# Kernel tuning notes

Measured on AMD Instinct MI355X. Metric: run time of the kernel, lower is better.

## Reference

```python
import jax, jax.numpy as jnp
import numpy as np

B, S, D, H = 16, 577, 768, 12  # batch, seq (24*24+1 cls), hidden, heads
WH, WW = 24, 24
HEAD = D // H
NUM_REL = (2 * WH - 1) * (2 * WW - 1) + 3  # 2212


def make_rel_pos_index(wh, ww):
    # mirrors TFData2VecVisionRelativePositionBias.get_position_index
    xx, yy = np.meshgrid(np.arange(wh), np.arange(ww))  # 'xy' indexing like tf.meshgrid
    coords = np.stack([yy, xx], axis=0).reshape(2, -1)  # [2, wh*ww]
    rel = coords[:, :, None] - coords[:, None, :]       # [2, N, N]
    rel = rel.transpose(1, 2, 0)                        # [N, N, 2]
    rx = (rel[:, :, 0] + wh - 1) * (2 * ww - 1)
    ry = rel[:, :, 1] + ww - 1
    idx = rx + ry                                       # [N, N]
    n = idx.shape[0]
    top = np.full((1, n), NUM_REL - 3, dtype=idx.dtype)
    left = np.full((n, 1), NUM_REL - 2, dtype=idx.dtype)
    corner = np.full((1, 1), NUM_REL - 1, dtype=idx.dtype)
    idx = np.concatenate([top, idx], axis=0)
    idx = np.concatenate([np.concatenate([corner, left], axis=0), idx], axis=1)
    return idx.astype(np.int32)  # [N+1, N+1]


def setup_inputs() -> dict:
    key = jax.random.key(0)
    ks = jax.random.split(key, 6)
    scale = 0.02
    return {
        "hidden_states": jax.random.normal(ks[0], (B, S, D), jnp.float32),
        "Wq": jax.random.normal(ks[1], (D, D), jnp.float32) * scale,
        "bq": jnp.zeros((D,), jnp.float32),
        "Wk": jax.random.normal(ks[2], (D, D), jnp.float32) * scale,
        "Wv": jax.random.normal(ks[3], (D, D), jnp.float32) * scale,
        "bv": jnp.zeros((D,), jnp.float32),
        "rel_pos_bias_table": jax.random.normal(ks[4], (NUM_REL, H), jnp.float32) * scale,
        "rel_pos_index": jnp.asarray(make_rel_pos_index(WH, WW)),
    }


def reference(hidden_states, Wq, bq, Wk, Wv, bv, rel_pos_bias_table, rel_pos_index):
    b, s, _ = hidden_states.shape
    q = (hidden_states @ Wq + bq).reshape(b, s, H, HEAD).transpose(0, 2, 1, 3)
    k = (hidden_states @ Wk).reshape(b, s, H, HEAD).transpose(0, 2, 1, 3)
    v = (hidden_states @ Wv + bv).reshape(b, s, H, HEAD).transpose(0, 2, 1, 3)
    scores = jnp.einsum("bhqd,bhkd->bhqk", q, k) / jnp.sqrt(jnp.float32(HEAD))
    # gathered relative position bias: [S, S, H] -> [H, S, S]
    bias = rel_pos_bias_table[rel_pos_index].transpose(2, 0, 1)
    scores = scores + bias[None]
    probs = jax.nn.softmax(scores, axis=-1)
    out = jnp.einsum("bhqk,bhkd->bhqd", probs, v)
    out = out.transpose(0, 2, 1, 3).reshape(b, s, D)
    return out
```

## Files before the change

kernel.cpp:

```cpp
#include <hip/hip_runtime.h>
#include <hip/hip_bf16.h>


typedef __attribute__((ext_vector_type(8))) short bf16x8;
typedef __attribute__((ext_vector_type(4))) float f32x4;
typedef unsigned short u16;

#define SEQ 577
#define MTOT 9232
#define QKV_STRIDE 7090176
#define VT_PITCH 640
#define B_PITCH 640

static __device__ __forceinline__ u16 f2bf(float x) {
  unsigned int u = __float_as_uint(x);
  u = (u + 0x7FFFu + ((u >> 16) & 1u)) >> 16;
  return (u16)u;
}
static __device__ __forceinline__ float bf2f(u16 v) {
  return __uint_as_float(((unsigned int)v) << 16);
}

static __device__ __forceinline__ void gload_lds16(const void* g, void* l) {
  __builtin_amdgcn_global_load_lds(
      (const __attribute__((address_space(1))) unsigned int*)g,
      (__attribute__((address_space(3))) unsigned int*)l, 16, 0, 0);
}

__global__ __launch_bounds__(256) void prep(
    const float* __restrict__ Wq, const float* __restrict__ Wk,
    const float* __restrict__ Wv, const float* __restrict__ X,
    u16* __restrict__ WT, u16* __restrict__ Xb) {
  const int bid = blockIdx.x;
  if (bid < 1728) {
    __shared__ float t[32][33];
    const int z = bid / 576;
    const int rem = bid - z * 576;
    const int kx = rem % 24, ny = rem / 24;
    const float* W = (z == 0) ? Wq : (z == 1) ? Wk : Wv;
    int x = threadIdx.x & 31;
    int y = threadIdx.x >> 5;
    int k0 = kx * 32;
    int n0 = ny * 32;
#pragma unroll
    for (int i = 0; i < 4; ++i)
      t[y + i * 8][x] = W[(size_t)(k0 + y + i * 8) * 768 + n0 + x];
    __syncthreads();
    u16* o = WT + (size_t)z * 589824;
#pragma unroll
    for (int i = 0; i < 4; ++i)
      o[(size_t)(n0 + y + i * 8) * 768 + k0 + x] = f2bf(t[x][y + i * 8]);
  } else {
    size_t i = ((size_t)(bid - 1728) * 256 + threadIdx.x) * 8;
    if (i >= (size_t)MTOT * 768) return;
    const float4* xp = (const float4*)(X + i);
    float4 a = xp[0], b = xp[1];
    u16 pk[8] = {f2bf(a.x), f2bf(a.y), f2bf(a.z), f2bf(a.w),
                 f2bf(b.x), f2bf(b.y), f2bf(b.z), f2bf(b.w)};
    *(int4*)(Xb + i) = *(const int4*)pk;
  }
}

__global__ __launch_bounds__(256) void prep2(
    const u16* __restrict__ v,
    u16* __restrict__ vT,
    const float* __restrict__ table, const int* __restrict__ idx,
    u16* __restrict__ biasm) {
  const int bid = blockIdx.x;
  const int tid = threadIdx.x;
  if (bid < 960) {
    const int tile = bid % 5;
    const int bh = bid / 5;
    const int b = bh / 12, h = bh % 12;
    __shared__ u16 T[128][64];
    const int s0 = tile * 128;
    const u16* vp = v + (size_t)b * SEQ * 768 + h * 64;
#pragma unroll
    for (int it = 0; it < 4; ++it) {
      int c = tid + it * 256;
      int r = c >> 3, ko = (c & 7) << 3;
      int gs = s0 + r;
      int4 val = make_int4(0, 0, 0, 0);
      if (gs < SEQ) val = *(const int4*)(vp + (size_t)gs * 768 + ko);
      *(int4*)&T[r][ko ^ (((r >> 3) & 7) << 3)] = val;
    }
    __syncthreads();
    u16* op = vT + (size_t)bh * 64 * VT_PITCH;
#pragma unroll
    for (int it = 0; it < 4; ++it) {
      int c = tid + it * 256;
      int d = c >> 4, so = (c & 15) << 3;
      u16 tmp[8];
#pragma unroll
      for (int j = 0; j < 8; ++j) {
        int rr = so + j;
        tmp[j] = T[rr][d ^ (((rr >> 3) & 7) << 3)];
      }
      *(int4*)(op + (size_t)d * VT_PITCH + s0 + so) = *(const int4*)tmp;
    }
  } else {
    const int r = bid - 960;
    const int q = r % 577;
    const int h = r / 577;
    for (int k = tid; k < B_PITCH; k += 256) {
      u16 vv = 0;
      if (k < SEQ) vv = f2bf(table[idx[q * SEQ + k] * 12 + h]);
      biasm[((size_t)h * SEQ + q) * B_PITCH + k] = vv;
    }
  }
}

#define STAGE_A(BUF, KT, MH)                                                   \
  do {                                                                         \
    gload_lds16(asrc[(MH)] + (KT) * 64, &TILES[(BUF)][0][(MH) * 64 + w8][0]);  \
    gload_lds16(asrc[(MH) + 2] + (KT) * 64,                                    \
                &TILES[(BUF)][0][128 + (MH) * 64 + w8][0]);                    \
  } while (0)

#define STAGE_B(BUF, KT, NH)                                                   \
  do {                                                                         \
    gload_lds16(bsrc + (size_t)((NH) * 32) * 768 + (KT) * 64,                  \
                &TILES[(BUF)][1][bw + (NH) * 32][0]);                          \
    gload_lds16(bsrc + (size_t)(128 + (NH) * 32) * 768 + (KT) * 64,            \
                &TILES[(BUF)][1][128 + bw + (NH) * 32][0]);                    \
  } while (0)

#define LOAD_A(BUF, MH)                                                        \
  do {                                                                         \
    const char* _p =                                                           \
        (const char*)&TILES[(BUF)][0][wm2 * 128 + (MH) * 64 + l15][0];         \
    af[0][0] = *(const bf16x8*)(_p + ca0);                                     \
    af[0][1] = *(const bf16x8*)(_p + ca1);                                     \
    af[1][0] = *(const bf16x8*)(_p + 2048 + ca0);                              \
    af[1][1] = *(const bf16x8*)(_p + 2048 + ca1);                              \
    af[2][0] = *(const bf16x8*)(_p + 4096 + ca0);                              \
    af[2][1] = *(const bf16x8*)(_p + 4096 + ca1);                              \
    af[3][0] = *(const bf16x8*)(_p + 6144 + ca0);                              \
    af[3][1] = *(const bf16x8*)(_p + 6144 + ca1);                              \
  } while (0)

#define LOAD_B(BUF, NH)                                                        \
  do {                                                                         \
    const char* _p =                                                           \
        (const char*)&TILES[(BUF)][1][wn * 64 + (NH) * 32 + l15][0];           \
    bfr[0][0] = *(const bf16x8*)(_p + ca0);                                    \
    bfr[0][1] = *(const bf16x8*)(_p + ca1);                                    \
    bfr[1][0] = *(const bf16x8*)(_p + 2048 + ca0);                             \
    bfr[1][1] = *(const bf16x8*)(_p + 2048 + ca1);                             \
  } while (0)

#define MFMA_Q(MH, NH)                                                         \
  do {                                                                         \
    _Pragma("unroll") for (int _i = 0; _i < 4; ++_i)                           \
        _Pragma("unroll") for (int _j = 0; _j < 2; ++_j)                       \
            acc[(MH) * 4 + _i][(NH) * 2 + _j] =                                \
        __builtin_amdgcn_mfma_f32_16x16x32_bf16(                               \
            af[_i][0], bfr[_j][0], acc[(MH) * 4 + _i][(NH) * 2 + _j], 0, 0,    \
            0);                                                                \
    _Pragma("unroll") for (int _i = 0; _i < 4; ++_i)                           \
        _Pragma("unroll") for (int _j = 0; _j < 2; ++_j)                       \
            acc[(MH) * 4 + _i][(NH) * 2 + _j] =                                \
        __builtin_amdgcn_mfma_f32_16x16x32_bf16(                               \
            af[_i][1], bfr[_j][1], acc[(MH) * 4 + _i][(NH) * 2 + _j], 0, 0,    \
            0);                                                                \
  } while (0)

#define PH_MID                                                                 \
  do {                                                                         \
    asm volatile("" ::: "memory");                                             \
    __builtin_amdgcn_s_barrier();                                              \
    asm volatile("s_waitcnt lgkmcnt(0)" ::: "memory");                         \
    __builtin_amdgcn_s_setprio(1);                                             \
  } while (0)

#define PH_END                                                                 \
  do {                                                                         \
    __builtin_amdgcn_s_setprio(0);                                             \
    asm volatile("" ::: "memory");                                             \
    __builtin_amdgcn_s_barrier();                                              \
    asm volatile("" ::: "memory");                                             \
  } while (0)

__global__ __launch_bounds__(512, 2) void qkv_gemm(
    const u16* __restrict__ Xb,
    const u16* __restrict__ WT,
    const float* __restrict__ bq, const float* __restrict__ bv,
    u16* __restrict__ qkv) {
  const int bid = blockIdx.x;
  const int xcd = bid & 7;
  const int r8 = bid >> 3;
  const int mt = (r8 / 9) * 8 + xcd;
  if (mt >= 37) return;
  const int nt = r8 % 9;
  const int m0 = mt * 256;
  const int widx = nt / 3;
  const int nb = (nt % 3) * 256;

  const int tid = threadIdx.x;
  const int lane = tid & 63;
  const int w = tid >> 6;
  const int wm2 = w >> 2;
  const int wn = w & 3;
  const int quad = lane >> 4;
  const int l15 = lane & 15;

  __shared__ u16 TILES[2][2][256][64];

  const int lr = lane >> 3;
  const int w8 = w * 8;
  const int ce = ((lane & 7) ^ lr) * 8;
  const u16* asrc[4];
#pragma unroll
  for (int c = 0; c < 4; ++c) {
    int rr = m0 + c * 64 + w8 + lr;
    if (rr > MTOT - 1) rr = MTOT - 1;
    asrc[c] = Xb + (size_t)rr * 768 + ce;
  }
  const int bw = (w >> 2) * 64 + (w & 3) * 8;
  const u16* bsrc = WT + (size_t)widx * 589824 + (size_t)(nb + bw + lr) * 768 + ce;

  const int lswz = (l15 & 7) << 4;
  const int ca0 = (quad * 16) ^ lswz;
  const int ca1 = ca0 ^ 64;

  f32x4 acc[8][4];
#pragma unroll
  for (int i = 0; i < 8; ++i)
#pragma unroll
    for (int j = 0; j < 4; ++j) acc[i][j] = (f32x4){0.f, 0.f, 0.f, 0.f};
  bf16x8 af[4][2], bfr[2][2];

  STAGE_A(0, 0, 0); STAGE_B(0, 0, 1); STAGE_A(0, 0, 1); STAGE_B(0, 0, 0);
  STAGE_A(1, 1, 0); STAGE_B(1, 1, 1); STAGE_A(1, 1, 1);
  asm volatile("s_waitcnt vmcnt(6)" ::: "memory");
  __builtin_amdgcn_s_barrier();
  asm volatile("" ::: "memory");

  for (int t = 0; t < 12; ++t) {
    const int buf = t & 1;
    const int nbuf = buf ^ 1;
    LOAD_A(buf, 0);
    LOAD_B(buf, 0);
    if (t <= 10) STAGE_B(nbuf, t + 1, 0);
    PH_MID; MFMA_Q(0, 0); PH_END;
    LOAD_B(buf, 1);
    if (t <= 9) STAGE_A(buf, t + 2, 0);
    PH_MID; MFMA_Q(0, 1); PH_END;
    LOAD_A(buf, 1);
    if (t <= 9) STAGE_B(buf, t + 2, 1);
    PH_MID; MFMA_Q(1, 1); PH_END;
    LOAD_B(buf, 0);
    if (t <= 9) STAGE_A(buf, t + 2, 1);
    asm volatile("" ::: "memory");
    __builtin_amdgcn_s_barrier();
    asm volatile("s_waitcnt lgkmcnt(0)" ::: "memory");
    __builtin_amdgcn_s_setprio(1);
    MFMA_Q(1, 0);
    __builtin_amdgcn_s_setprio(0);
    if (t < 10) {
      asm volatile("s_waitcnt vmcnt(6)" ::: "memory");
    } else if (t == 10) {
      asm volatile("s_waitcnt vmcnt(0)" ::: "memory");
    }
    asm volatile("" ::: "memory");
    __builtin_amdgcn_s_barrier();
    asm volatile("" ::: "memory");
  }

  const float scale = (widx == 0) ? 0.125f : 1.0f;
  float biasv[4];
#pragma unroll
  for (int nf = 0; nf < 4; ++nf) {
    int n = nb + wn * 64 + nf * 16 + l15;
    biasv[nf] = (widx == 0) ? bq[n] * 0.125f : (widx == 2) ? bv[n] : 0.f;
  }
  u16* E = (u16*)TILES;
#pragma unroll
  for (int mf = 0; mf < 8; ++mf)
#pragma unroll
    for (int nf = 0; nf < 4; ++nf)
#pragma unroll
      for (int rr = 0; rr < 4; ++rr) {
        int rowl = wm2 * 128 + mf * 16 + quad * 4 + rr;
        int col = wn * 64 + nf * 16 + l15;
        E[rowl * 256 + (col ^ (quad << 4))] =
            f2bf(acc[mf][nf][rr] * scale + biasv[nf]);
      }
  __syncthreads();
  u16* ob = qkv + (size_t)widx * QKV_STRIDE + nb;
#pragma unroll 4
  for (int pass = 0; pass < 16; ++pass) {
    int c = pass * 512 + tid;
    int row = c >> 5, ch = c & 31;
    int m = m0 + row;
    if (m < MTOT) {
      int colr = (ch * 8) ^ (((row >> 2) & 3) << 4);
      *(int4*)(ob + (size_t)m * 768 + ch * 8) = *(const int4*)&E[row * 256 + colr];
    }
  }
}

__global__ __launch_bounds__(512) void attn(
    const u16* __restrict__ qk, const u16* __restrict__ vT,
    const u16* __restrict__ biasm, float* __restrict__ out) {
  const int bh = blockIdx.x;
  const int qt = blockIdx.y;
  const int b = bh / 12, h = bh - b * 12;
  const int tid = threadIdx.x;
  const int lane = tid & 63;
  const int w = tid >> 6;
  const int quad = lane >> 4;
  const int l15 = lane & 15;

  const u16* qp = qk + (size_t)b * SEQ * 768 + h * 64;
  const u16* kp = qp + (size_t)QKV_STRIDE;
  const u16* vtp = vT + (size_t)bh * 64 * VT_PITCH;
  const u16* bp = biasm + (size_t)h * SEQ * B_PITCH;

  __shared__ u16 Ks[64][72];
  __shared__ u16 VTs[64][72];
  __shared__ u16 Ps[8][16][72];

  const int qrow0 = qt * 128 + w * 16;

  bf16x8 qf[2];
  {
    int row = qrow0 + l15;
    if (row > 576) row = 576;
    qf[0] = *(const bf16x8*)(qp + (size_t)row * 768 + quad * 8);
    qf[1] = *(const bf16x8*)(qp + (size_t)row * 768 + 32 + quad * 8);
  }
  int brow[4];
#pragma unroll
  for (int r = 0; r < 4; ++r) {
    int rr = qrow0 + quad * 4 + r;
    if (rr > 576) rr = 576;
    brow[r] = rr;
  }

  float lacc[4] = {0.f, 0.f, 0.f, 0.f};
  f32x4 O[4];
#pragma unroll
  for (int dt = 0; dt < 4; ++dt) O[dt] = (f32x4){0.f, 0.f, 0.f, 0.f};

  for (int kt = 0; kt < 10; ++kt) {
    const int kbase = kt * 64;
    u16 bb[4][4];
#pragma unroll
    for (int nt = 0; nt < 4; ++nt)
#pragma unroll
      for (int r = 0; r < 4; ++r)
        bb[nt][r] = bp[(size_t)brow[r] * B_PITCH + kbase + nt * 16 + l15];

    {
      int rr = tid >> 3, ko = (tid & 7) << 3;
      int gk = kbase + rr;
      int4 kvv = make_int4(0, 0, 0, 0);
      if (gk < SEQ) kvv = *(const int4*)(kp + (size_t)gk * 768 + ko);
      *(int4*)&Ks[rr][ko] = kvv;
      *(int4*)&VTs[rr][ko] = *(const int4*)(vtp + (size_t)rr * VT_PITCH + kbase + ko);
    }
    __syncthreads();

    f32x4 s[4];
#pragma unroll
    for (int nt = 0; nt < 4; ++nt) {
      f32x4 z = (f32x4){bf2f(bb[nt][0]), bf2f(bb[nt][1]),
                        bf2f(bb[nt][2]), bf2f(bb[nt][3])};
      bf16x8 kf0 = *(const bf16x8*)(&Ks[nt * 16 + l15][quad * 8]);
      bf16x8 kf1 = *(const bf16x8*)(&Ks[nt * 16 + l15][32 + quad * 8]);
      z = __builtin_amdgcn_mfma_f32_16x16x32_bf16(qf[0], kf0, z, 0, 0, 0);
      z = __builtin_amdgcn_mfma_f32_16x16x32_bf16(qf[1], kf1, z, 0, 0, 0);
      s[nt] = z;
    }

    const bool full = (kbase + 64 <= SEQ);
#pragma unroll
    for (int nt = 0; nt < 4; ++nt) {
#pragma unroll
      for (int r = 0; r < 4; ++r) {
        float p = __expf(s[nt][r]);
        unsigned int u = __float_as_uint(p);
        float pt = __uint_as_float(u & 0xFFFF0000u);
        if (full) lacc[r] += pt;
        else lacc[r] += ((kbase + nt * 16 + l15) < SEQ) ? pt : 0.f;
        Ps[w][quad * 4 + r][((nt ^ quad) << 4) + l15] = (u16)(u >> 16);
      }
    }

#pragma unroll
    for (int ks = 0; ks < 2; ++ks) {
      int cc = (ks * 32 + quad * 8) ^ ((l15 >> 2) << 4);
      bf16x8 pf = *(const bf16x8*)(&Ps[w][l15][cc]);
#pragma unroll
      for (int dt = 0; dt < 4; ++dt) {
        bf16x8 vf = *(const bf16x8*)(&VTs[dt * 16 + l15][ks * 32 + quad * 8]);
        O[dt] = __builtin_amdgcn_mfma_f32_16x16x32_bf16(pf, vf, O[dt], 0, 0, 0);
      }
    }
    __syncthreads();
  }

#pragma unroll
  for (int r = 0; r < 4; ++r) {
    float l = lacc[r];
    l += __shfl_xor(l, 1);
    l += __shfl_xor(l, 2);
    l += __shfl_xor(l, 4);
    l += __shfl_xor(l, 8);
    int row = qrow0 + quad * 4 + r;
    if (row < SEQ) {
      float inv = 1.f / l;
#pragma unroll
      for (int dt = 0; dt < 4; ++dt)
        out[((size_t)(b * SEQ + row)) * 768 + h * 64 + dt * 16 + l15] = O[dt][r] * inv;
    }
  }
}

extern "C" void kernel_launch(void* const* d_in, const int* in_sizes, int n_in,
                              void* d_out, int out_size, void* d_ws, size_t ws_size,
                              hipStream_t stream) {
  const float* hs = (const float*)d_in[0];
  const float* Wq = (const float*)d_in[1];
  const float* bq = (const float*)d_in[2];
  const float* Wk = (const float*)d_in[3];
  const float* Wv = (const float*)d_in[4];
  const float* bv = (const float*)d_in[5];
  const float* table = (const float*)d_in[6];
  const int* idx = (const int*)d_in[7];
  float* out = (float*)d_out;

  char* ws = (char*)d_ws;
  u16* qkv = (u16*)ws;
  u16* WT = (u16*)(ws + 42541056);
  u16* Xb = (u16*)(ws + 46080000);
  u16* vT = (u16*)(ws + 42541056);
  u16* biasm = (u16*)(ws + 58269696);

  hipLaunchKernelGGL(prep, dim3(5190), dim3(256), 0, stream, Wq, Wk, Wv, hs, WT, Xb);
  hipLaunchKernelGGL(qkv_gemm, dim3(360), dim3(512), 0, stream, Xb, WT, bq, bv, qkv);
  hipLaunchKernelGGL(prep2, dim3(7884), dim3(256), 0, stream,
                     qkv + 2 * (size_t)QKV_STRIDE, vT, table, idx, biasm);
  hipLaunchKernelGGL(attn, dim3(192, 5), dim3(512), 0, stream, qkv, vT, biasm, out);
}
```

Measured before the change: 201.6 us.

## Fold log2e into Q scale and bias, compute row sums via MFMA

Pre-scales Q by log2(e)/8 and the gathered bias table by log2(e), so the softmax can use exp2 directly. Padded bias columns are set to a large negative value, which makes padded keys contribute roughly zero and removes per-element masking. The per-lane row-sum accumulation and cross-lane shuffles are replaced by an extra MFMA of P against a ones vector. The bias-prep kernel now gathers all 12 heads per query row with vectorized table loads, cutting its grid from 7884 to 1537 blocks.

```diff
diff --git a/kernel.cpp b/kernel.cpp
--- a/kernel.cpp
+++ b/kernel.cpp
@@ -11,6 +11,8 @@
 #define QKV_STRIDE 7090176
 #define VT_PITCH 640
 #define B_PITCH 640
+#define QSCALE 0.18033688f
+#define LOG2E 1.44269504f
 
 static __device__ __forceinline__ u16 f2bf(float x) {
   unsigned int u = __float_as_uint(x);
@@ -99,13 +101,27 @@
       *(int4*)(op + (size_t)d * VT_PITCH + s0 + so) = *(const int4*)tmp;
     }
   } else {
-    const int r = bid - 960;
-    const int q = r % 577;
-    const int h = r / 577;
+    const int q = bid - 960;
+    const int* idxq = idx + q * SEQ;
+    const u16 pad = f2bf(-144.0f);
     for (int k = tid; k < B_PITCH; k += 256) {
-      u16 vv = 0;
-      if (k < SEQ) vv = f2bf(table[idx[q * SEQ + k] * 12 + h]);
-      biasm[((size_t)h * SEQ + q) * B_PITCH + k] = vv;
+      u16 vv[12];
+      if (k < SEQ) {
+        const float4* tp = (const float4*)(table + (size_t)idxq[k] * 12);
+        float4 t0 = tp[0], t1 = tp[1], t2 = tp[2];
+        vv[0] = f2bf(t0.x * LOG2E);  vv[1] = f2bf(t0.y * LOG2E);
+        vv[2] = f2bf(t0.z * LOG2E);  vv[3] = f2bf(t0.w * LOG2E);
+        vv[4] = f2bf(t1.x * LOG2E);  vv[5] = f2bf(t1.y * LOG2E);
+        vv[6] = f2bf(t1.z * LOG2E);  vv[7] = f2bf(t1.w * LOG2E);
+        vv[8] = f2bf(t2.x * LOG2E);  vv[9] = f2bf(t2.y * LOG2E);
+        vv[10] = f2bf(t2.z * LOG2E); vv[11] = f2bf(t2.w * LOG2E);
+      } else {
+#pragma unroll
+        for (int h = 0; h < 12; ++h) vv[h] = pad;
+      }
+#pragma unroll
+      for (int h = 0; h < 12; ++h)
+        biasm[((size_t)h * SEQ + q) * B_PITCH + k] = vv[h];
     }
   }
 }
@@ -267,12 +283,12 @@
     asm volatile("" ::: "memory");
   }
 
-  const float scale = (widx == 0) ? 0.125f : 1.0f;
+  const float scale = (widx == 0) ? QSCALE : 1.0f;
   float biasv[4];
 #pragma unroll
   for (int nf = 0; nf < 4; ++nf) {
     int n = nb + wn * 64 + nf * 16 + l15;
-    biasv[nf] = (widx == 0) ? bq[n] * 0.125f : (widx == 2) ? bv[n] : 0.f;
+    biasv[nf] = (widx == 0) ? bq[n] * QSCALE : (widx == 2) ? bv[n] : 0.f;
   }
   u16* E = (u16*)TILES;
 #pragma unroll
@@ -338,7 +354,11 @@
     brow[r] = rr;
   }
 
-  float lacc[4] = {0.f, 0.f, 0.f, 0.f};
+  const short one_bf = (short)0x3F80;
+  const bf16x8 vones = {one_bf, one_bf, one_bf, one_bf,
+                        one_bf, one_bf, one_bf, one_bf};
+
+  f32x4 Ol = (f32x4){0.f, 0.f, 0.f, 0.f};
   f32x4 O[4];
 #pragma unroll
   for (int dt = 0; dt < 4; ++dt) O[dt] = (f32x4){0.f, 0.f, 0.f, 0.f};
@@ -374,16 +394,12 @@
       s[nt] = z;
     }
 
-    const bool full = (kbase + 64 <= SEQ);
 #pragma unroll
     for (int nt = 0; nt < 4; ++nt) {
 #pragma unroll
       for (int r = 0; r < 4; ++r) {
-        float p = __expf(s[nt][r]);
+        float p = exp2f(s[nt][r]);
         unsigned int u = __float_as_uint(p);
-        float pt = __uint_as_float(u & 0xFFFF0000u);
-        if (full) lacc[r] += pt;
-        else lacc[r] += ((kbase + nt * 16 + l15) < SEQ) ? pt : 0.f;
         Ps[w][quad * 4 + r][((nt ^ quad) << 4) + l15] = (u16)(u >> 16);
       }
     }
@@ -397,20 +413,16 @@
         bf16x8 vf = *(const bf16x8*)(&VTs[dt * 16 + l15][ks * 32 + quad * 8]);
         O[dt] = __builtin_amdgcn_mfma_f32_16x16x32_bf16(pf, vf, O[dt], 0, 0, 0);
       }
+      Ol = __builtin_amdgcn_mfma_f32_16x16x32_bf16(pf, vones, Ol, 0, 0, 0);
     }
     __syncthreads();
   }
 
 #pragma unroll
   for (int r = 0; r < 4; ++r) {
-    float l = lacc[r];
-    l += __shfl_xor(l, 1);
-    l += __shfl_xor(l, 2);
-    l += __shfl_xor(l, 4);
-    l += __shfl_xor(l, 8);
     int row = qrow0 + quad * 4 + r;
     if (row < SEQ) {
-      float inv = 1.f / l;
+      float inv = 1.f / Ol[r];
 #pragma unroll
       for (int dt = 0; dt < 4; ++dt)
         out[((size_t)(b * SEQ + row)) * 768 + h * 64 + dt * 16 + l15] = O[dt][r] * inv;
@@ -440,7 +452,7 @@
 
   hipLaunchKernelGGL(prep, dim3(5190), dim3(256), 0, stream, Wq, Wk, Wv, hs, WT, Xb);
   hipLaunchKernelGGL(qkv_gemm, dim3(360), dim3(512), 0, stream, Xb, WT, bq, bv, qkv);
-  hipLaunchKernelGGL(prep2, dim3(7884), dim3(256), 0, stream,
+  hipLaunchKernelGGL(prep2, dim3(1537), dim3(256), 0, stream,
                      qkv + 2 * (size_t)QKV_STRIDE, vT, table, idx, biasm);
   hipLaunchKernelGGL(attn, dim3(192, 5), dim3(512), 0, stream, qkv, vT, biasm, out);
 }
```

Measured after the change: 203.2 us. About the same (+0.8%).
